# Kernel tuning notes

Measured on AMD Instinct MI355X. Metric: run time of the kernel, lower is better.

Reference implementation:

```python
import jax, jax.numpy as jnp
import numpy as np

N, D, H, O, E, K = 4096, 512, 1024, 512, 8, 2


def setup_inputs() -> dict:
    key = jax.random.key(0)
    ks = jax.random.split(key, 7)
    s = 0.02
    return {
        "x": jax.random.normal(ks[0], (N, D), dtype=jnp.float32),
        "W1": jax.random.normal(ks[1], (E, D, H), dtype=jnp.float32) * s,
        "b1": jnp.zeros((E, H), dtype=jnp.float32),
        "W2": jax.random.normal(ks[2], (E, H, O), dtype=jnp.float32) * s,
        "b2": jnp.zeros((E, O), dtype=jnp.float32),
        "Wg": jax.random.normal(ks[3], (D, E), dtype=jnp.float32) * s,
        "bg": jnp.zeros((E,), dtype=jnp.float32),
        "k": K,
    }


def reference(x, W1, b1, W2, b2, Wg, bg, k):
    # Gating: softmax over experts, then top-k with renormalized weights
    gates = jax.nn.softmax(x @ Wg + bg, axis=1)              # [N, E]
    topv, topi = jax.lax.top_k(gates, k)                     # [N, k]
    w = topv / jnp.sum(topv, axis=1, keepdims=True)          # renormalized top-k weights

    # Dense per-expert two-layer MLP (grouped GEMM form)
    h = jax.nn.relu(jnp.einsum('nd,edh->neh', x, W1) + b1[None])   # [N, E, H]
    y = jnp.einsum('neh,eho->neo', h, W2) + b2[None]               # [N, E, O]

    # Gather selected experts and combine
    y_sel = jnp.take_along_axis(y, topi[:, :, None], axis=1)       # [N, k, O]
    out = jnp.einsum('nko,nk->no', y_sel, w)                       # [N, O]
    return out, gates, topi
```

## Files before the change

### kernel.cpp

```cpp
#include <hip/hip_runtime.h>
#include <hip/hip_bf16.h>

#define N_TOK 4096
#define DIM   512
#define HID   1024
#define OUTD  512
#define NEXP  8
#define TOPK  2

#define MT1 72
#define HROWS 9216
#define L1B (MT1 * 8)

typedef __bf16 bf16;
typedef bf16  bf16x8 __attribute__((ext_vector_type(8)));
typedef bf16  bf16x4 __attribute__((ext_vector_type(4)));
typedef float f32x4  __attribute__((ext_vector_type(4)));

__device__ inline f32x4 mfma16(bf16x8 a, bf16x8 b, f32x4 c) {
    return __builtin_amdgcn_mfma_f32_16x16x32_bf16(a, b, c, 0, 0, 0);
}

__device__ inline void gload16(const bf16* g, char* l) {
    __builtin_amdgcn_global_load_lds(
        (const __attribute__((address_space(1))) void*)g,
        (__attribute__((address_space(3))) void*)l, 16, 0, 0);
}

__device__ inline void transpose32(const float* __restrict__ s, bf16* __restrict__ d,
                                   int C, int R, int c0, int r0, char* ldsb, int tid)
{
    float (*tile)[33] = (float(*)[33])ldsb;
    int tx = tid & 31, ty = tid >> 5;
#pragma unroll
    for (int i = 0; i < 4; ++i)
        tile[ty + i * 8][tx] = s[(size_t)(r0 + ty + i * 8) * C + c0 + tx];
    __syncthreads();
    int dc = tid >> 3, q = tid & 7;
    bf16x4 v;
#pragma unroll
    for (int j = 0; j < 4; ++j) v[j] = (bf16)tile[q * 4 + j][dc];
    *(bf16x4*)(d + (size_t)(c0 + dc) * R + r0 + q * 4) = v;
}

__global__ __launch_bounds__(256) void w1gate_kernel(
    const float* __restrict__ W1, const float* __restrict__ Wg,
    const float* __restrict__ bg, const float* __restrict__ x,
    bf16* __restrict__ W1t, bf16* __restrict__ xb,
    float* __restrict__ gates_out, float* __restrict__ topi_out,
    int* __restrict__ pick_e, float* __restrict__ pick_w)
{
    __shared__ __align__(16) float smem[NEXP * DIM];
    int b = blockIdx.x;

    if (b >= 4096) {
        const float4* Wg4 = (const float4*)Wg;
        for (int i = threadIdx.x; i < DIM * NEXP / 4; i += 256) {
            float4 v = Wg4[i];
#pragma unroll
            for (int j = 0; j < 4; ++j) {
                int idx = i * 4 + j;
                smem[(idx & 7) * DIM + (idx >> 3)] = ((const float*)&v)[j];
            }
        }
        __syncthreads();

        int wave = threadIdx.x >> 6;
        int lane = threadIdx.x & 63;
        int n = (b - 4096) * 4 + wave;

        const float4* x4 = (const float4*)(x + (size_t)n * DIM);
        float4 v0 = x4[lane];
        float4 v1 = x4[lane + 64];

        bf16x4 o0 = { (bf16)v0.x, (bf16)v0.y, (bf16)v0.z, (bf16)v0.w };
        bf16x4 o1 = { (bf16)v1.x, (bf16)v1.y, (bf16)v1.z, (bf16)v1.w };
        bf16x4* xb4 = (bf16x4*)(xb + (size_t)n * DIM);
        xb4[lane]      = o0;
        xb4[lane + 64] = o1;

        float acc[NEXP];
#pragma unroll
        for (int e = 0; e < NEXP; ++e) {
            const float4* wr = (const float4*)(smem + e * DIM);
            float4 w0 = wr[lane];
            float4 w1 = wr[lane + 64];
            acc[e] = v0.x * w0.x + v0.y * w0.y + v0.z * w0.z + v0.w * w0.w
                   + v1.x * w1.x + v1.y * w1.y + v1.z * w1.z + v1.w * w1.w;
        }
#pragma unroll
        for (int off = 32; off >= 1; off >>= 1) {
#pragma unroll
            for (int e = 0; e < NEXP; ++e) acc[e] += __shfl_xor(acc[e], off, 64);
        }
#pragma unroll
        for (int e = 0; e < NEXP; ++e) acc[e] += bg[e];

        float m = acc[0];
#pragma unroll
        for (int e = 1; e < NEXP; ++e) m = fmaxf(m, acc[e]);
        float g[NEXP];
        float s = 0.f;
#pragma unroll
        for (int e = 0; e < NEXP; ++e) { g[e] = expf(acc[e] - m); s += g[e]; }
        float inv_s = 1.f / s;
#pragma unroll
        for (int e = 0; e < NEXP; ++e) g[e] *= inv_s;

        if (lane < NEXP) gates_out[n * NEXP + lane] = g[lane];

        if (lane == 0) {
            int m1 = 0;
#pragma unroll
            for (int e = 1; e < NEXP; ++e) if (g[e] > g[m1]) m1 = e;
            int m2 = (m1 == 0) ? 1 : 0;
#pragma unroll
            for (int e = 0; e < NEXP; ++e) if (e != m1 && g[e] > g[m2]) m2 = e;
            float v1g = g[m1], v2g = g[m2];
            float inv = 1.f / (v1g + v2g);
            topi_out[n * TOPK + 0] = (float)m1;
            topi_out[n * TOPK + 1] = (float)m2;
            int2 pe = { m1, m2 };
            float2 pw = { v1g * inv, v2g * inv };
            *(int2*)(pick_e + n * 2) = pe;
            *(float2*)(pick_w + n * 2) = pw;
        }
        return;
    }

    int e = b >> 9, rem = b & 511;
    transpose32(W1 + (size_t)e * DIM * HID, W1t + (size_t)e * DIM * HID,
                HID, DIM, (rem & 31) * 32, (rem >> 5) * 32, (char*)smem, threadIdx.x);
}

__global__ __launch_bounds__(1024) void bucket_sched_kernel(
    const int* __restrict__ pick_e,
    int* __restrict__ counts, int* __restrict__ tlist, int* __restrict__ meta)
{
    __shared__ int cnt[NEXP];
    if (threadIdx.x < NEXP) cnt[threadIdx.x] = 0;
    __syncthreads();
    for (int i = threadIdx.x; i < N_TOK * 2; i += 1024) {
        int e = pick_e[i];
        int p = atomicAdd(&cnt[e], 1);
        tlist[e * N_TOK + p] = i;
    }
    __syncthreads();
    if (threadIdx.x == 0) {
        int base = 0, t1 = 0;
        for (int e = 0; e < NEXP; ++e) {
            int c = cnt[e];
            counts[e] = c;
            int n1 = (c + 127) >> 7;
            for (int lt = 0; lt < n1; ++lt) {
                meta[2 + t1 * 3]     = e;
                meta[2 + t1 * 3 + 1] = base + lt * 128;
                meta[2 + t1 * 3 + 2] = lt * 128;
                ++t1;
            }
            base += n1 << 7;
        }
        meta[0] = t1;
    }
}


__global__ __launch_bounds__(256, 4) void l1_kernel(
    const bf16* __restrict__ xb, const bf16* __restrict__ W1t,
    const float* __restrict__ b1, const int* __restrict__ counts,
    const int* __restrict__ tlist, const int* __restrict__ meta,
    bf16* __restrict__ h,
    const float* __restrict__ W2, bf16* __restrict__ W2t)
{
    __shared__ __align__(16) char lds[32768];
    int bid = blockIdx.x, tid = threadIdx.x;

    if (bid >= L1B) {
        int t = bid - L1B;
        int e = t >> 9, rem = t & 511;
        transpose32(W2 + (size_t)e * HID * OUTD, W2t + (size_t)e * HID * OUTD,
                    OUTD, HID, (rem & 15) * 32, (rem >> 4) * 32, lds, tid);
        return;
    }

    int mt = bid >> 3, nt = bid & 7;
    if (mt >= meta[0]) return;
    const int* s1 = meta + 2 + mt * 3;
    int e = s1[0], rb = s1[1], i0 = s1[2];
    int cnt = counts[e];

    int w = tid >> 6, l = tid & 63;
    int c0 = w * 128 + l, c1 = c0 + 64;
    int rA0 = c0 >> 2, rA1 = c1 >> 2;
    int kA0 = (c0 & 3) ^ ((rA0 & 3) ^ ((rA0 >> 2) & 1));
    int kA1 = (c1 & 3) ^ ((rA1 & 3) ^ ((rA1 >> 2) & 1));
    int iA0 = i0 + rA0, iA1 = i0 + rA1;
    const int* tl = tlist + e * N_TOK;
    int tok0 = iA0 < cnt ? (tl[iA0] >> 1) : 0;
    int tok1 = iA1 < cnt ? (tl[iA1] >> 1) : 0;
    const bf16* sA0 = xb + (size_t)tok0 * DIM + kA0 * 8;
    const bf16* sA1 = xb + (size_t)tok1 * DIM + kA1 * 8;
    int n0 = nt * 128;
    const bf16* w1e = W1t + (size_t)e * HID * DIM;
    const bf16* sB0 = w1e + (size_t)(n0 + rA0) * DIM + kA0 * 8;
    const bf16* sB1 = w1e + (size_t)(n0 + rA1) * DIM + kA1 * 8;
    int oA0 = c0 * 16, oA1 = c1 * 16;

    f32x4 acc[4][4];
#pragma unroll
    for (int mf = 0; mf < 4; ++mf)
#pragma unroll
        for (int nf = 0; nf < 4; ++nf) acc[mf][nf] = (f32x4){0.f, 0.f, 0.f, 0.f};

    int wm = w >> 1, wn = w & 1;
    int lr = l & 15;
    int kb = ((l >> 4) ^ ((l & 3) ^ ((l >> 2) & 1))) * 16;

    {
        char* A = lds;       char* B = lds + 8192;
        gload16(sA0, A + oA0); gload16(sA1, A + oA1);
        gload16(sB0, B + oA0); gload16(sB1, B + oA1);
    }

    for (int ks = 0; ks < 16; ++ks) {
        __syncthreads();
        if (ks < 15) {
            char* A = lds + (((ks + 1) & 1) * 16384);
            char* B = A + 8192;
            int kof = (ks + 1) * 32;
            gload16(sA0 + kof, A + oA0); gload16(sA1 + kof, A + oA1);
            gload16(sB0 + kof, B + oA0); gload16(sB1 + kof, B + oA1);
        }
        char* A = lds + ((ks & 1) * 16384);
        char* B = A + 8192;
        bf16x8 af[4], bfr[4];
#pragma unroll
        for (int mf = 0; mf < 4; ++mf)
            af[mf] = *(const bf16x8*)(A + (wm * 64 + mf * 16 + lr) * 64 + kb);
#pragma unroll
        for (int nf = 0; nf < 4; ++nf)
            bfr[nf] = *(const bf16x8*)(B + (wn * 64 + nf * 16 + lr) * 64 + kb);
#pragma unroll
        for (int mf = 0; mf < 4; ++mf)
#pragma unroll
            for (int nf = 0; nf < 4; ++nf)
                acc[mf][nf] = mfma16(af[mf], bfr[nf], acc[mf][nf]);
    }

    __syncthreads();
    bf16* ct = (bf16*)lds;
    const float* b1e = b1 + e * HID;
#pragma unroll
    for (int nf = 0; nf < 4; ++nf) {
        int col = wn * 64 + nf * 16 + lr;
        float bias = b1e[n0 + col];
#pragma unroll
        for (int mf = 0; mf < 4; ++mf) {
#pragma unroll
            for (int r = 0; r < 4; ++r) {
                int row = wm * 64 + mf * 16 + (l >> 4) * 4 + r;
                float v = fmaxf(acc[mf][nf][r] + bias, 0.f);
                int g = (col >> 3) ^ (row & 3);
                ct[row * 128 + g * 8 + (col & 7)] = (bf16)v;
            }
        }
    }
    __syncthreads();
#pragma unroll
    for (int p = 0; p < 8; ++p) {
        int row = p * 16 + (tid >> 4);
        int ch = tid & 15;
        int g = ch ^ (row & 3);
        bf16x8 v = *(const bf16x8*)(ct + row * 128 + g * 8);
        *(bf16x8*)(h + (size_t)(rb + row) * HID + n0 + ch * 8) = v;
    }
}

__global__ __launch_bounds__(256, 4) void l2_kernel(
    const bf16* __restrict__ h, const bf16* __restrict__ W2t,
    const int* __restrict__ counts, const int* __restrict__ tlist,
    const int* __restrict__ meta, bf16* __restrict__ ybuf)
{
    int mt = blockIdx.x >> 2, nt = blockIdx.x & 3;
    if (mt >= meta[0]) return;
    const int* s1 = meta + 2 + mt * 3;
    int e = s1[0], rb = s1[1], i0 = s1[2];
    int cnt = counts[e];

    __shared__ __align__(16) char lds[32768];

    int tid = threadIdx.x, w = tid >> 6, l = tid & 63;
    int c0 = w * 128 + l, c1 = c0 + 64;
    int rA0 = c0 >> 2, rA1 = c1 >> 2;
    int kA0 = (c0 & 3) ^ ((rA0 & 3) ^ ((rA0 >> 2) & 1));
    int kA1 = (c1 & 3) ^ ((rA1 & 3) ^ ((rA1 >> 2) & 1));
    const bf16* sA0 = h + (size_t)(rb + rA0) * HID + kA0 * 8;
    const bf16* sA1 = h + (size_t)(rb + rA1) * HID + kA1 * 8;
    int n0 = nt * 128;
    const bf16* w2e = W2t + (size_t)e * OUTD * HID;
    const bf16* sB0 = w2e + (size_t)(n0 + rA0) * HID + kA0 * 8;
    const bf16* sB1 = w2e + (size_t)(n0 + rA1) * HID + kA1 * 8;
    int oA0 = c0 * 16, oA1 = c1 * 16;

    f32x4 acc[4][4];
#pragma unroll
    for (int mf = 0; mf < 4; ++mf)
#pragma unroll
        for (int nf = 0; nf < 4; ++nf) acc[mf][nf] = (f32x4){0.f, 0.f, 0.f, 0.f};

    int wm = w >> 1, wn = w & 1;
    int lr = l & 15;
    int kb = ((l >> 4) ^ ((l & 3) ^ ((l >> 2) & 1))) * 16;

    {
        char* A = lds;       char* B = lds + 8192;
        gload16(sA0, A + oA0); gload16(sA1, A + oA1);
        gload16(sB0, B + oA0); gload16(sB1, B + oA1);
    }

    for (int ks = 0; ks < 32; ++ks) {
        __syncthreads();
        if (ks < 31) {
            char* A = lds + (((ks + 1) & 1) * 16384);
            char* B = A + 8192;
            int kof = (ks + 1) * 32;
            gload16(sA0 + kof, A + oA0); gload16(sA1 + kof, A + oA1);
            gload16(sB0 + kof, B + oA0); gload16(sB1 + kof, B + oA1);
        }
        char* A = lds + ((ks & 1) * 16384);
        char* B = A + 8192;
        bf16x8 af[4], bfr[4];
#pragma unroll
        for (int mf = 0; mf < 4; ++mf)
            af[mf] = *(const bf16x8*)(A + (wm * 64 + mf * 16 + lr) * 64 + kb);
#pragma unroll
        for (int nf = 0; nf < 4; ++nf)
            bfr[nf] = *(const bf16x8*)(B + (wn * 64 + nf * 16 + lr) * 64 + kb);
#pragma unroll
        for (int mf = 0; mf < 4; ++mf)
#pragma unroll
            for (int nf = 0; nf < 4; ++nf)
                acc[mf][nf] = mfma16(af[mf], bfr[nf], acc[mf][nf]);
    }

    __syncthreads();
    bf16* ct = (bf16*)lds;
#pragma unroll
    for (int nf = 0; nf < 4; ++nf) {
        int col = wn * 64 + nf * 16 + lr;
#pragma unroll
        for (int mf = 0; mf < 4; ++mf) {
#pragma unroll
            for (int r = 0; r < 4; ++r) {
                int row = wm * 64 + mf * 16 + (l >> 4) * 4 + r;
                int g = (col >> 3) ^ (row & 3);
                ct[row * 128 + g * 8 + (col & 7)] = (bf16)acc[mf][nf][r];
            }
        }
    }
    __syncthreads();
    const int* tl = tlist + e * N_TOK;
#pragma unroll
    for (int p = 0; p < 8; ++p) {
        int row = p * 16 + (tid >> 4);
        int i = i0 + row;
        if (i < cnt) {
            int pi = tl[i];
            int ch = tid & 15;
            int g = ch ^ (row & 3);
            bf16x8 v = *(const bf16x8*)(ct + row * 128 + g * 8);
            *(bf16x8*)(ybuf + (size_t)pi * OUTD + n0 + ch * 8) = v;
        }
    }
}

__global__ __launch_bounds__(256) void combine_kernel(
    const bf16* __restrict__ ybuf, const float* __restrict__ b2,
    const int* __restrict__ pick_e, const float* __restrict__ pick_w,
    float* __restrict__ out)
{
    int wave = threadIdx.x >> 6;
    int lane = threadIdx.x & 63;
    int n = blockIdx.x * 4 + wave;

    int e0 = pick_e[n * 2], e1 = pick_e[n * 2 + 1];
    float w0 = pick_w[n * 2], w1 = pick_w[n * 2 + 1];

    const bf16x8* y0 = (const bf16x8*)(ybuf + (size_t)(n * 2) * OUTD);
    const bf16x8* y1 = (const bf16x8*)(ybuf + (size_t)(n * 2 + 1) * OUTD);
    const float4* b20 = (const float4*)(b2 + e0 * OUTD);
    const float4* b21 = (const float4*)(b2 + e1 * OUTD);
    float4* o4 = (float4*)(out + (size_t)n * OUTD);

    bf16x8 a = y0[lane];
    bf16x8 b = y1[lane];
    float4 c0 = b20[lane * 2], c1 = b20[lane * 2 + 1];
    float4 d0 = b21[lane * 2], d1 = b21[lane * 2 + 1];

    float4 r0, r1;
    r0.x = w0 * ((float)a[0] + c0.x) + w1 * ((float)b[0] + d0.x);
    r0.y = w0 * ((float)a[1] + c0.y) + w1 * ((float)b[1] + d0.y);
    r0.z = w0 * ((float)a[2] + c0.z) + w1 * ((float)b[2] + d0.z);
    r0.w = w0 * ((float)a[3] + c0.w) + w1 * ((float)b[3] + d0.w);
    r1.x = w0 * ((float)a[4] + c1.x) + w1 * ((float)b[4] + d1.x);
    r1.y = w0 * ((float)a[5] + c1.y) + w1 * ((float)b[5] + d1.y);
    r1.z = w0 * ((float)a[6] + c1.z) + w1 * ((float)b[6] + d1.z);
    r1.w = w0 * ((float)a[7] + c1.w) + w1 * ((float)b[7] + d1.w);
    o4[lane * 2]     = r0;
    o4[lane * 2 + 1] = r1;
}

extern "C" void kernel_launch(void* const* d_in, const int* in_sizes, int n_in,
                              void* d_out, int out_size, void* d_ws, size_t ws_size,
                              hipStream_t stream)
{
    const float* x  = (const float*)d_in[0];
    const float* W1 = (const float*)d_in[1];
    const float* b1 = (const float*)d_in[2];
    const float* W2 = (const float*)d_in[3];
    const float* b2 = (const float*)d_in[4];
    const float* Wg = (const float*)d_in[5];
    const float* bg = (const float*)d_in[6];

    float* out_f   = (float*)d_out;
    float* gates_o = out_f + (size_t)N_TOK * OUTD;
    float* topi_o  = gates_o + (size_t)N_TOK * NEXP;

    char* ws = (char*)d_ws;
    size_t offW1t = 0;
    size_t offW2t = offW1t + (size_t)NEXP * HID * DIM * 2;
    size_t offXb  = offW2t + (size_t)NEXP * OUTD * HID * 2;
    size_t offH   = offXb + (size_t)N_TOK * DIM * 2;
    size_t offYb  = offH + (size_t)HROWS * HID * 2;
    size_t offCnt = offYb + (size_t)N_TOK * 2 * OUTD * 2;
    size_t offTl  = offCnt + 256;
    size_t offMeta = offTl + (size_t)NEXP * N_TOK * 4;
    size_t offPkE = offMeta + 4096;
    size_t offPkW = offPkE + (size_t)N_TOK * 2 * 4;

    bf16*  W1t    = (bf16*)(ws + offW1t);
    bf16*  W2t    = (bf16*)(ws + offW2t);
    bf16*  xbuf   = (bf16*)(ws + offXb);
    bf16*  hbuf   = (bf16*)(ws + offH);
    bf16*  ybuf   = (bf16*)(ws + offYb);
    int*   cnts   = (int*)(ws + offCnt);
    int*   tlist  = (int*)(ws + offTl);
    int*   meta   = (int*)(ws + offMeta);
    int*   pick_e = (int*)(ws + offPkE);
    float* pick_w = (float*)(ws + offPkW);

    w1gate_kernel<<<4096 + N_TOK / 4, 256, 0, stream>>>(
        W1, Wg, bg, x, W1t, xbuf, gates_o, topi_o, pick_e, pick_w);

    bucket_sched_kernel<<<1, 1024, 0, stream>>>(pick_e, cnts, tlist, meta);

    l1_kernel<<<L1B + 4096, 256, 0, stream>>>(
        xbuf, W1t, b1, cnts, tlist, meta, hbuf, W2, W2t);

    l2_kernel<<<MT1 * 4, 256, 0, stream>>>(hbuf, W2t, cnts, tlist, meta, ybuf);

    combine_kernel<<<N_TOK / 4, 256, 0, stream>>>(ybuf, b2, pick_e, pick_w, out_f);
}
```

Baseline: 75.40 us.

## Split gating from W1 transpose and overlap bucket scheduling with transpose

```diff
diff --git a/kernel.cpp b/kernel.cpp
--- a/kernel.cpp
+++ b/kernel.cpp
@@ -43,125 +43,127 @@
     *(bf16x4*)(d + (size_t)(c0 + dc) * R + r0 + q * 4) = v;
 }
 
-__global__ __launch_bounds__(256) void w1gate_kernel(
-    const float* __restrict__ W1, const float* __restrict__ Wg,
-    const float* __restrict__ bg, const float* __restrict__ x,
-    bf16* __restrict__ W1t, bf16* __restrict__ xb,
+__global__ __launch_bounds__(256) void gate_kernel(
+    const float* __restrict__ Wg, const float* __restrict__ bg,
+    const float* __restrict__ x, bf16* __restrict__ xb,
     float* __restrict__ gates_out, float* __restrict__ topi_out,
     int* __restrict__ pick_e, float* __restrict__ pick_w)
 {
     __shared__ __align__(16) float smem[NEXP * DIM];
-    int b = blockIdx.x;
-
-    if (b >= 4096) {
-        const float4* Wg4 = (const float4*)Wg;
-        for (int i = threadIdx.x; i < DIM * NEXP / 4; i += 256) {
-            float4 v = Wg4[i];
-#pragma unroll
-            for (int j = 0; j < 4; ++j) {
-                int idx = i * 4 + j;
-                smem[(idx & 7) * DIM + (idx >> 3)] = ((const float*)&v)[j];
+    const float4* Wg4 = (const float4*)Wg;
+    for (int i = threadIdx.x; i < DIM * NEXP / 4; i += 256) {
+        float4 v = Wg4[i];
+#pragma unroll
+        for (int j = 0; j < 4; ++j) {
+            int idx = i * 4 + j;
+            smem[(idx & 7) * DIM + (idx >> 3)] = ((const float*)&v)[j];
+        }
+    }
+    __syncthreads();
+
+    int wave = threadIdx.x >> 6;
+    int lane = threadIdx.x & 63;
+    int n = blockIdx.x * 4 + wave;
+
+    const float4* x4 = (const float4*)(x + (size_t)n * DIM);
+    float4 v0 = x4[lane];
+    float4 v1 = x4[lane + 64];
+
+    bf16x4 o0 = { (bf16)v0.x, (bf16)v0.y, (bf16)v0.z, (bf16)v0.w };
+    bf16x4 o1 = { (bf16)v1.x, (bf16)v1.y, (bf16)v1.z, (bf16)v1.w };
+    bf16x4* xb4 = (bf16x4*)(xb + (size_t)n * DIM);
+    xb4[lane]      = o0;
+    xb4[lane + 64] = o1;
+
+    float acc[NEXP];
+#pragma unroll
+    for (int e = 0; e < NEXP; ++e) {
+        const float4* wr = (const float4*)(smem + e * DIM);
+        float4 w0 = wr[lane];
+        float4 w1 = wr[lane + 64];
+        acc[e] = v0.x * w0.x + v0.y * w0.y + v0.z * w0.z + v0.w * w0.w
+               + v1.x * w1.x + v1.y * w1.y + v1.z * w1.z + v1.w * w1.w;
+    }
+#pragma unroll
+    for (int off = 32; off >= 1; off >>= 1) {
+#pragma unroll
+        for (int e = 0; e < NEXP; ++e) acc[e] += __shfl_xor(acc[e], off, 64);
+    }
+#pragma unroll
+    for (int e = 0; e < NEXP; ++e) acc[e] += bg[e];
+
+    float m = acc[0];
+#pragma unroll
+    for (int e = 1; e < NEXP; ++e) m = fmaxf(m, acc[e]);
+    float g[NEXP];
+    float s = 0.f;
+#pragma unroll
+    for (int e = 0; e < NEXP; ++e) { g[e] = expf(acc[e] - m); s += g[e]; }
+    float inv_s = 1.f / s;
+#pragma unroll
+    for (int e = 0; e < NEXP; ++e) g[e] *= inv_s;
+
+    if (lane < NEXP) gates_out[n * NEXP + lane] = g[lane];
+
+    if (lane == 0) {
+        int m1 = 0;
+#pragma unroll
+        for (int e = 1; e < NEXP; ++e) if (g[e] > g[m1]) m1 = e;
+        int m2 = (m1 == 0) ? 1 : 0;
+#pragma unroll
+        for (int e = 0; e < NEXP; ++e) if (e != m1 && g[e] > g[m2]) m2 = e;
+        float v1g = g[m1], v2g = g[m2];
+        float inv = 1.f / (v1g + v2g);
+        topi_out[n * TOPK + 0] = (float)m1;
+        topi_out[n * TOPK + 1] = (float)m2;
+        int2 pe = { m1, m2 };
+        float2 pw = { v1g * inv, v2g * inv };
+        *(int2*)(pick_e + n * 2) = pe;
+        *(float2*)(pick_w + n * 2) = pw;
+    }
+}
+
+__global__ __launch_bounds__(256) void w1t_bucket_kernel(
+    const float* __restrict__ W1, const int* __restrict__ pick_e,
+    bf16* __restrict__ W1t,
+    int* __restrict__ counts, int* __restrict__ tlist, int* __restrict__ meta)
+{
+    __shared__ __align__(16) float smem[NEXP * DIM];
+    int b = blockIdx.x, tid = threadIdx.x;
+
+    if (b == 0) {
+        __shared__ int cnt[NEXP];
+        if (tid < NEXP) cnt[tid] = 0;
+        __syncthreads();
+        for (int i = tid; i < N_TOK * 2; i += 256) {
+            int e = pick_e[i];
+            int p = atomicAdd(&cnt[e], 1);
+            tlist[e * N_TOK + p] = i;
+        }
+        __syncthreads();
+        if (tid == 0) {
+            int base = 0, t1 = 0;
+            for (int e = 0; e < NEXP; ++e) {
+                int c = cnt[e];
+                counts[e] = c;
+                int n1 = (c + 127) >> 7;
+                for (int lt = 0; lt < n1; ++lt) {
+                    meta[2 + t1 * 3]     = e;
+                    meta[2 + t1 * 3 + 1] = base + lt * 128;
+                    meta[2 + t1 * 3 + 2] = lt * 128;
+                    ++t1;
+                }
+                base += n1 << 7;
             }
-        }
-        __syncthreads();
-
-        int wave = threadIdx.x >> 6;
-        int lane = threadIdx.x & 63;
-        int n = (b - 4096) * 4 + wave;
-
-        const float4* x4 = (const float4*)(x + (size_t)n * DIM);
-        float4 v0 = x4[lane];
-        float4 v1 = x4[lane + 64];
-
-        bf16x4 o0 = { (bf16)v0.x, (bf16)v0.y, (bf16)v0.z, (bf16)v0.w };
-        bf16x4 o1 = { (bf16)v1.x, (bf16)v1.y, (bf16)v1.z, (bf16)v1.w };
-        bf16x4* xb4 = (bf16x4*)(xb + (size_t)n * DIM);
-        xb4[lane]      = o0;
-        xb4[lane + 64] = o1;
-
-        float acc[NEXP];
-#pragma unroll
-        for (int e = 0; e < NEXP; ++e) {
-            const float4* wr = (const float4*)(smem + e * DIM);
-            float4 w0 = wr[lane];
-            float4 w1 = wr[lane + 64];
-            acc[e] = v0.x * w0.x + v0.y * w0.y + v0.z * w0.z + v0.w * w0.w
-                   + v1.x * w1.x + v1.y * w1.y + v1.z * w1.z + v1.w * w1.w;
-        }
-#pragma unroll
-        for (int off = 32; off >= 1; off >>= 1) {
-#pragma unroll
-            for (int e = 0; e < NEXP; ++e) acc[e] += __shfl_xor(acc[e], off, 64);
-        }
-#pragma unroll
-        for (int e = 0; e < NEXP; ++e) acc[e] += bg[e];
-
-        float m = acc[0];
-#pragma unroll
-        for (int e = 1; e < NEXP; ++e) m = fmaxf(m, acc[e]);
-        float g[NEXP];
-        float s = 0.f;
-#pragma unroll
-        for (int e = 0; e < NEXP; ++e) { g[e] = expf(acc[e] - m); s += g[e]; }
-        float inv_s = 1.f / s;
-#pragma unroll
-        for (int e = 0; e < NEXP; ++e) g[e] *= inv_s;
-
-        if (lane < NEXP) gates_out[n * NEXP + lane] = g[lane];
-
-        if (lane == 0) {
-            int m1 = 0;
-#pragma unroll
-            for (int e = 1; e < NEXP; ++e) if (g[e] > g[m1]) m1 = e;
-            int m2 = (m1 == 0) ? 1 : 0;
-#pragma unroll
-            for (int e = 0; e < NEXP; ++e) if (e != m1 && g[e] > g[m2]) m2 = e;
-            float v1g = g[m1], v2g = g[m2];
-            float inv = 1.f / (v1g + v2g);
-            topi_out[n * TOPK + 0] = (float)m1;
-            topi_out[n * TOPK + 1] = (float)m2;
-            int2 pe = { m1, m2 };
-            float2 pw = { v1g * inv, v2g * inv };
-            *(int2*)(pick_e + n * 2) = pe;
-            *(float2*)(pick_w + n * 2) = pw;
+            meta[0] = t1;
         }
         return;
     }
 
-    int e = b >> 9, rem = b & 511;
+    int t = b - 1;
+    int e = t >> 9, rem = t & 511;
     transpose32(W1 + (size_t)e * DIM * HID, W1t + (size_t)e * DIM * HID,
-                HID, DIM, (rem & 31) * 32, (rem >> 5) * 32, (char*)smem, threadIdx.x);
-}
-
-__global__ __launch_bounds__(1024) void bucket_sched_kernel(
-    const int* __restrict__ pick_e,
-    int* __restrict__ counts, int* __restrict__ tlist, int* __restrict__ meta)
-{
-    __shared__ int cnt[NEXP];
-    if (threadIdx.x < NEXP) cnt[threadIdx.x] = 0;
-    __syncthreads();
-    for (int i = threadIdx.x; i < N_TOK * 2; i += 1024) {
-        int e = pick_e[i];
-        int p = atomicAdd(&cnt[e], 1);
-        tlist[e * N_TOK + p] = i;
-    }
-    __syncthreads();
-    if (threadIdx.x == 0) {
-        int base = 0, t1 = 0;
-        for (int e = 0; e < NEXP; ++e) {
-            int c = cnt[e];
-            counts[e] = c;
-            int n1 = (c + 127) >> 7;
-            for (int lt = 0; lt < n1; ++lt) {
-                meta[2 + t1 * 3]     = e;
-                meta[2 + t1 * 3 + 1] = base + lt * 128;
-                meta[2 + t1 * 3 + 2] = lt * 128;
-                ++t1;
-            }
-            base += n1 << 7;
-        }
-        meta[0] = t1;
-    }
+                HID, DIM, (rem & 31) * 32, (rem >> 5) * 32, (char*)smem, tid);
 }
 
 
@@ -449,10 +451,11 @@
     int*   pick_e = (int*)(ws + offPkE);
     float* pick_w = (float*)(ws + offPkW);
 
-    w1gate_kernel<<<4096 + N_TOK / 4, 256, 0, stream>>>(
-        W1, Wg, bg, x, W1t, xbuf, gates_o, topi_o, pick_e, pick_w);
-
-    bucket_sched_kernel<<<1, 1024, 0, stream>>>(pick_e, cnts, tlist, meta);
+    gate_kernel<<<N_TOK / 4, 256, 0, stream>>>(
+        Wg, bg, x, xbuf, gates_o, topi_o, pick_e, pick_w);
+
+    w1t_bucket_kernel<<<4097, 256, 0, stream>>>(
+        W1, pick_e, W1t, cnts, tlist, meta);
 
     l1_kernel<<<L1B + 4096, 256, 0, stream>>>(
         xbuf, W1t, b1, cnts, tlist, meta, hbuf, W2, W2t);
```

New measurement: 78.88 us. 4.6% more time.
